# Kernel optimization log

Measured on AMD Instinct MI355X. Metric: run time of the kernel, lower is better.

## Reference

```python
import jax, jax.numpy as jnp
import numpy as np
from jax import lax

FEAT_STRIDE = 16
SCALES = (8.0, 16.0, 32.0)
RATIOS = (0.5, 1.0, 2.0)
PRE_NMS_TOPN = 6000
POST_NMS_TOPN = 300
NMS_THRESH = 0.5
MIN_SIZE = 16.0


def _generate_anchors(base_size=16.0):
    # Faithful Caffe generate_anchors: ratio enumeration outer, scale inner.
    w = h = base_size
    x_ctr = y_ctr = (base_size - 1.0) / 2.0
    size = w * h
    anchors = []
    for r in RATIOS:
        ws = np.round(np.sqrt(size / r))
        hs = np.round(ws * r)
        for s in SCALES:
            W = ws * s
            H = hs * s
            anchors.append([x_ctr - (W - 1) / 2.0, y_ctr - (H - 1) / 2.0,
                            x_ctr + (W - 1) / 2.0, y_ctr + (H - 1) / 2.0])
    return np.asarray(anchors, dtype=np.float32)  # (A=9, 4)


def _nms_keep(boxes, thresh):
    # boxes sorted by descending score; returns bool keep mask. JIT-friendly.
    n = boxes.shape[0]
    x1, y1, x2, y2 = boxes[:, 0], boxes[:, 1], boxes[:, 2], boxes[:, 3]
    areas = (x2 - x1 + 1.0) * (y2 - y1 + 1.0)
    xx1 = jnp.maximum(x1[:, None], x1[None, :])
    yy1 = jnp.maximum(y1[:, None], y1[None, :])
    xx2 = jnp.minimum(x2[:, None], x2[None, :])
    yy2 = jnp.minimum(y2[:, None], y2[None, :])
    inter = jnp.maximum(xx2 - xx1 + 1.0, 0.0) * jnp.maximum(yy2 - yy1 + 1.0, 0.0)
    iou = inter / (areas[:, None] + areas[None, :] - inter)  # (n, n)
    idxs = jnp.arange(n)

    def body(i, keep):
        suppress = (iou[i] > thresh) & keep[i] & (idxs > i)
        return keep & ~suppress

    return lax.fori_loop(0, n, body, jnp.ones((n,), dtype=bool))


def _proposal(scores, bbox_deltas):
    # scores: (1, H, W, 2A) rpn class probs; bbox_deltas: (1, H, W, 4A)
    _, H, W, A4 = bbox_deltas.shape
    A = A4 // 4
    im_h = jnp.float32(H * FEAT_STRIDE)
    im_w = jnp.float32(W * FEAT_STRIDE)

    anchors = jnp.asarray(_generate_anchors())  # (A, 4)
    shift_x = jnp.arange(W, dtype=jnp.float32) * FEAT_STRIDE
    shift_y = jnp.arange(H, dtype=jnp.float32) * FEAT_STRIDE
    sx, sy = jnp.meshgrid(shift_x, shift_y)  # (H, W) row-major like Caffe
    shifts = jnp.stack([sx.ravel(), sy.ravel(), sx.ravel(), sy.ravel()], axis=1)  # (K, 4)
    all_anchors = (anchors[None, :, :] + shifts[:, None, :]).reshape(-1, 4)  # (K*A, 4)

    fg_scores = scores[0, :, :, A:].reshape(-1)        # (K*A,) fg probs
    deltas = bbox_deltas[0].reshape(-1, 4)             # (K*A, 4)

    # bbox_transform_inv (Caffe convention with +1 widths)
    aw = all_anchors[:, 2] - all_anchors[:, 0] + 1.0
    ah = all_anchors[:, 3] - all_anchors[:, 1] + 1.0
    acx = all_anchors[:, 0] + 0.5 * aw
    acy = all_anchors[:, 1] + 0.5 * ah
    dx, dy, dw, dh = deltas[:, 0], deltas[:, 1], deltas[:, 2], deltas[:, 3]
    pcx = dx * aw + acx
    pcy = dy * ah + acy
    pw = jnp.exp(dw) * aw
    ph = jnp.exp(dh) * ah
    x1 = jnp.clip(pcx - 0.5 * pw, 0.0, im_w - 1.0)
    y1 = jnp.clip(pcy - 0.5 * ph, 0.0, im_h - 1.0)
    x2 = jnp.clip(pcx + 0.5 * pw, 0.0, im_w - 1.0)
    y2 = jnp.clip(pcy + 0.5 * ph, 0.0, im_h - 1.0)
    proposals = jnp.stack([x1, y1, x2, y2], axis=1)  # (K*A, 4)

    # min_size filter (im scale = 1): mask score to -inf instead of removing
    ws = x2 - x1 + 1.0
    hs = y2 - y1 + 1.0
    valid = (ws >= MIN_SIZE) & (hs >= MIN_SIZE)
    masked_scores = jnp.where(valid, fg_scores, -jnp.inf)

    top_scores, order = lax.top_k(masked_scores, PRE_NMS_TOPN)
    top_boxes = proposals[order]  # (pre_nms, 4), score-descending

    keep = _nms_keep(lax.stop_gradient(top_boxes), NMS_THRESH)
    keep = keep & jnp.isfinite(top_scores)

    n = PRE_NMS_TOPN
    ranked = jnp.where(keep, jnp.arange(n), n)
    picked = jnp.sort(ranked)[:POST_NMS_TOPN]  # first kept in score order
    ok = picked < n
    picked_c = jnp.minimum(picked, n - 1)
    out_boxes = top_boxes[picked_c] * ok[:, None].astype(top_boxes.dtype)

    # normalized proposals in [0, 1]
    scale = jnp.array([im_w, im_h, im_w, im_h], dtype=top_boxes.dtype)
    return out_boxes / scale  # (post_nms_topN, 4)


def setup_inputs() -> dict:
    key = jax.random.key(0)
    k1, k2 = jax.random.split(key)
    scores = jax.random.uniform(k1, (1, 64, 64, 18), dtype=jnp.float32)
    bbox_deltas = jax.random.normal(k2, (1, 64, 64, 36), dtype=jnp.float32)
    return {"scores": scores, "bbox_deltas": bbox_deltas}


def reference(scores, bbox_deltas):
    return _proposal(scores, bbox_deltas)
```

## Files before the change

### kernel.cpp

```cpp
#include <hip/hip_runtime.h>
#include <math.h>


#define NPROP   36864
#define TOPN    6000
#define POSTN   300
#define NWORDS  94
#define NROUND  47
#define MAXSEL  8192
#define NB      16384
#define NEGINF_PAT 0x007FFFFFu

typedef unsigned long long u64;

__constant__ float ANCH[9][4] = {
    {-84.f,  -40.f,  99.f,  55.f},
    {-176.f, -88.f,  191.f, 103.f},
    {-360.f, -184.f, 375.f, 199.f},
    {-56.f,  -56.f,  71.f,  71.f},
    {-120.f, -120.f, 135.f, 135.f},
    {-248.f, -248.f, 263.f, 263.f},
    {-36.f,  -80.f,  51.f,  95.f},
    {-80.f,  -168.f, 95.f,  183.f},
    {-168.f, -344.f, 183.f, 359.f},
};

__device__ __forceinline__ float4 decode_box(const float* __restrict__ deltas, int i,
                                             bool* valid_out) {
    int a   = i % 9;
    int pos = i / 9;
    int wx = pos & 63, hy = pos >> 6;
    float sx = (float)(wx * 16), sy = (float)(hy * 16);
    float ax1 = ANCH[a][0] + sx, ay1 = ANCH[a][1] + sy;
    float ax2 = ANCH[a][2] + sx, ay2 = ANCH[a][3] + sy;
    float aw  = ax2 - ax1 + 1.0f;
    float ah  = ay2 - ay1 + 1.0f;
    float acx = ax1 + 0.5f * aw;
    float acy = ay1 + 0.5f * ah;
    float4 d4 = ((const float4*)deltas)[i];
    float pcx = __fadd_rn(__fmul_rn(d4.x, aw), acx);
    float pcy = __fadd_rn(__fmul_rn(d4.y, ah), acy);
    float pw  = __fmul_rn(expf(d4.z), aw);
    float ph  = __fmul_rn(expf(d4.w), ah);
    float hx  = __fmul_rn(0.5f, pw);
    float hv  = __fmul_rn(0.5f, ph);
    float x1 = fminf(fmaxf(__fsub_rn(pcx, hx), 0.0f), 1023.0f);
    float y1 = fminf(fmaxf(__fsub_rn(pcy, hv), 0.0f), 1023.0f);
    float x2 = fminf(fmaxf(__fadd_rn(pcx, hx), 0.0f), 1023.0f);
    float y2 = fminf(fmaxf(__fadd_rn(pcy, hv), 0.0f), 1023.0f);
    float bw = __fadd_rn(__fsub_rn(x2, x1), 1.0f);
    float bh = __fadd_rn(__fsub_rn(y2, y1), 1.0f);
    *valid_out = (bw >= 16.0f) && (bh >= 16.0f);
    return make_float4(x1, y1, x2, y2);
}

__device__ __forceinline__ float box_area(float4 b) {
    return __fmul_rn(__fadd_rn(__fsub_rn(b.z, b.x), 1.0f),
                     __fadd_rn(__fsub_rn(b.w, b.y), 1.0f));
}

__global__ __launch_bounds__(256) void decode_kernel(
        const float* __restrict__ scores,
        const float* __restrict__ deltas,
        unsigned* __restrict__ uhigh) {
    int i = blockIdx.x * 256 + threadIdx.x;
    bool valid;
    (void)decode_box(deltas, i, &valid);
    int a = i % 9, pos = i / 9;
    float fg = scores[(size_t)pos * 18 + 9 + a];
    float sc = valid ? fg : -__builtin_huge_valf();
    unsigned u = __float_as_uint(sc);
    u = (u & 0x80000000u) ? ~u : (u | 0x80000000u);
    uhigh[i] = u;
}

__global__ __launch_bounds__(1024) void select_compact(
        const unsigned* __restrict__ uhigh,
        u64* __restrict__ sel,
        unsigned* __restrict__ nsel) {
    __shared__ unsigned h[NB];
    __shared__ unsigned strip[1024];
    __shared__ unsigned thr_sh, cnt_sh;
    int t = threadIdx.x, lane = t & 63, wave = t >> 6;
    #pragma unroll
    for (int r = 0; r < NB / 1024; ++r) h[t + r * 1024] = 0;
    if (t == 0) cnt_sh = 0;
    __syncthreads();

    #pragma unroll
    for (int r = 0; r < 36; ++r) {
        unsigned u = uhigh[t + r * 1024];
        unsigned bkt = u >> 18;
        atomicAdd(&h[(bkt >> 4) + (bkt & 15) * 1024], 1u);
    }
    __syncthreads();

    unsigned s = 0;
    #pragma unroll
    for (int k = 0; k < 16; ++k) s += h[t + k * 1024];
    strip[t] = s;
    __syncthreads();

    if (wave == 0) {
        unsigned g = 0;
        #pragma unroll
        for (int k = 0; k < 16; ++k) g += strip[lane * 16 + k];
        unsigned suf = g;
        #pragma unroll
        for (int off = 1; off < 64; off <<= 1) {
            unsigned x = __shfl_down(suf, off, 64);
            if (lane + off < 64) suf += x;
        }
        u64 bal = __ballot(suf >= TOPN);
        int gsel = 63 - __builtin_clzll(bal);
        unsigned rest = __shfl(suf, (gsel < 63) ? gsel + 1 : 63, 64);
        if (gsel == 63) rest = 0;

        unsigned sv = (lane < 16) ? strip[gsel * 16 + lane] : 0;
        unsigned suf2 = sv;
        #pragma unroll
        for (int off = 1; off < 16; off <<= 1) {
            unsigned x = __shfl_down(suf2, off, 64);
            if (lane + off < 16) suf2 += x;
        }
        u64 bal2 = __ballot((lane < 16) && (rest + suf2 >= TOPN));
        int ssel = 63 - __builtin_clzll(bal2);
        unsigned rest2 = __shfl(suf2, (ssel < 15) ? ssel + 1 : 15, 64);
        if (ssel == 15) rest2 = 0;
        rest2 += rest;
        int S = gsel * 16 + ssel;

        unsigned bv = (lane < 16) ? h[S + lane * 1024] : 0;
        unsigned suf3 = bv;
        #pragma unroll
        for (int off = 1; off < 16; off <<= 1) {
            unsigned x = __shfl_down(suf3, off, 64);
            if (lane + off < 16) suf3 += x;
        }
        u64 bal3 = __ballot((lane < 16) && (rest2 + suf3 >= TOPN));
        int bsel = 63 - __builtin_clzll(bal3);
        if (lane == 0) thr_sh = ((unsigned)(S * 16 + bsel)) << 18;
    }
    __syncthreads();
    unsigned thr = thr_sh;

    for (int r = 0; r < 36; ++r) {
        unsigned u = uhigh[t + r * 1024];
        bool pred = (u >= thr);
        u64 b = __ballot(pred);
        int nb = __popcll(b);
        unsigned base = 0;
        if (lane == 0 && nb) base = atomicAdd(&cnt_sh, (unsigned)nb);
        base = __shfl(base, 0, 64);
        if (pred) {
            unsigned p = base + (unsigned)__popcll(b & ((1ULL << lane) - 1ULL));
            if (p < MAXSEL)
                sel[p] = ((u64)u << 32) |
                         (u64)(0xFFFFFFFFu - (unsigned)(t + r * 1024));
        }
    }
    __syncthreads();
    if (t == 0) *nsel = (cnt_sh > MAXSEL) ? MAXSEL : cnt_sh;
}

__global__ __launch_bounds__(256) void rank_scatter(
        const u64* __restrict__ sel,
        const unsigned* __restrict__ nsel,
        const float* __restrict__ deltas,
        float4* __restrict__ topb,
        float* __restrict__ areas,
        unsigned* __restrict__ topu) {
    __shared__ u64 tile[1024];
    __shared__ int pr[256];
    int t = threadIdx.x;
    int slot = t & 31, seg = t >> 5;
    int n = (int)*nsel; if (n > MAXSEL) n = MAXSEL;
    int j = blockIdx.x * 32 + slot;
    u64 myk = (j < n) ? sel[j] : 0ULL;
    int rk = 0;
    for (int base = 0; base < n; base += 1024) {
        int m = min(1024, n - base);
        for (int q = t; q < m; q += 256) tile[q] = sel[base + q];
        __syncthreads();
        for (int q = seg; q < m; q += 8) rk += (tile[q] > myk) ? 1 : 0;
        __syncthreads();
    }
    pr[seg * 32 + slot] = rk;
    __syncthreads();
    if (t < 32) {
        int jj = blockIdx.x * 32 + t;
        int rtot = 0;
        #pragma unroll
        for (int s2 = 0; s2 < 8; ++s2) rtot += pr[s2 * 32 + t];
        if (jj < n && rtot < TOPN) {
            u64 k = sel[jj];
            unsigned idx = 0xFFFFFFFFu - (unsigned)(k & 0xFFFFFFFFull);
            bool valid;
            float4 b = decode_box(deltas, (int)idx, &valid);
            topb[rtot]  = b;
            areas[rtot] = box_area(b);
            topu[rtot]  = (unsigned)(k >> 32);
        }
    }
}

__global__ void nms_mask(const float4* __restrict__ boxes,
                         const float* __restrict__ areas,
                         u64* __restrict__ mask) {
    int rb = blockIdx.x, cb = blockIdx.y;
    if (cb < rb) return;
    __shared__ float4 cbx[64];
    __shared__ float  car[64];
    int tid = threadIdx.x;
    int j0 = cb * 64;
    if (j0 + tid < TOPN) { cbx[tid] = boxes[j0 + tid]; car[tid] = areas[j0 + tid]; }
    __syncthreads();
    int i = rb * 64 + tid;
    if (i >= TOPN) return;
    float4 bi = boxes[i];
    float  ai = areas[i];
    u64 bits = 0ULL;
    int jmax = min(64, TOPN - j0);
    for (int jj = 0; jj < jmax; ++jj) {
        int j = j0 + jj;
        if (j <= i) continue;
        float4 bj = cbx[jj];
        float xx1 = fmaxf(bi.x, bj.x);
        float yy1 = fmaxf(bi.y, bj.y);
        float xx2 = fminf(bi.z, bj.z);
        float yy2 = fminf(bi.w, bj.w);
        float w = fmaxf(__fadd_rn(__fsub_rn(xx2, xx1), 1.0f), 0.0f);
        float h = fmaxf(__fadd_rn(__fsub_rn(yy2, yy1), 1.0f), 0.0f);
        float inter = __fmul_rn(w, h);
        float denom = __fsub_rn(__fadd_rn(ai, car[jj]), inter);
        float iou = inter / denom;
        if (iou > 0.5f) bits |= (1ULL << jj);
    }
    mask[(size_t)i * NWORDS + cb] = bits;
}

__global__ __launch_bounds__(1024) void nms_scan(
        const u64* __restrict__ mask,
        const unsigned* __restrict__ topu,
        const float4* __restrict__ topb,
        float* __restrict__ out) {
    __shared__ unsigned rem32[NWORDS * 2];
    __shared__ u64 diag[2][128][4];
    __shared__ u64 Fsh[2][2];
    __shared__ short kept_rows[2][128];
    __shared__ short kept_list[POSTN];
    __shared__ int nk_sh[2];
    __shared__ int cnt_sh, stop_sh;

    int t = threadIdx.x, wave = t >> 6, lane = t & 63;
    if (t >= 640 && t < 640 + NWORDS * 2) rem32[t - 640] = 0;
    if (t >= 128 && t < 640) {
        int idx = t - 128;
        diag[0][idx >> 2][idx & 3] = mask[(size_t)(idx >> 2) * NWORDS + (idx & 3)];
    }
    if (wave == 0) {
        u64 f = __ballot(topu[lane] != NEGINF_PAT);
        if (lane == 0) { Fsh[0][0] = f; cnt_sh = 0; stop_sh = 0; nk_sh[0] = 0; nk_sh[1] = 0; }
    } else if (wave == 1) {
        u64 f = __ballot(topu[64 + lane] != NEGINF_PAT);
        if (lane == 0) Fsh[0][1] = f;
    }
    __syncthreads();

    u64 urg0 = 0, urg1 = 0;

    for (int r = 0; r < NROUND; ++r) {
        int p = r & 1;
        int i0 = r * 128;
        if (wave == 0) {
            u64 r0w0 = diag[p][lane][0];
            u64 r0w1 = diag[p][lane][1];
            u64 r1w1 = diag[p][64 + lane][1];
            u64 R0 = ((u64)rem32[4 * r]     | ((u64)rem32[4 * r + 1] << 32)) | urg0;
            u64 R1 = ((u64)rem32[4 * r + 2] | ((u64)rem32[4 * r + 3] << 32)) | urg1;
            int nb = min(128, TOPN - i0);
            u64 v1 = (nb >= 128) ? ~0ULL : ((1ULL << (nb - 64)) - 1ULL);
            u64 a0 = ~R0;
            u64 a1 = ~R1 & v1;
            u64 k0 = 0ULL, k1 = 0ULL;
            while (a0) {
                int ii = __builtin_ctzll(a0);
                u64 bit = 1ULL << ii;
                k0 |= bit;
                u64 s0 = __shfl(r0w0, ii, 64);
                u64 s1 = __shfl(r0w1, ii, 64);
                a0 &= ~(s0 | bit);
                a1 &= ~s1;
            }
            while (a1) {
                int ii = __builtin_ctzll(a1);
                u64 bit = 1ULL << ii;
                k1 |= bit;
                u64 s1 = __shfl(r1w1, ii, 64);
                a1 &= ~(s1 | bit);
            }
            u64 F0 = Fsh[p][0], F1 = Fsh[p][1];
            u64 kf0 = k0 & F0, kf1 = k1 & F1;
            int nk0 = __popcll(k0);
            int c0  = __popcll(kf0);
            int base = cnt_sh;
            u64 ltm = (1ULL << lane) - 1ULL;
            if ((k0 >> lane) & 1)
                kept_rows[p][__popcll(k0 & ltm)] = (short)(i0 + lane);
            if ((k1 >> lane) & 1)
                kept_rows[p][nk0 + __popcll(k1 & ltm)] = (short)(i0 + 64 + lane);
            if ((kf0 >> lane) & 1) {
                int pos = base + __popcll(kf0 & ltm);
                if (pos < POSTN) kept_list[pos] = (short)(i0 + lane);
            }
            if ((kf1 >> lane) & 1) {
                int pos = base + c0 + __popcll(kf1 & ltm);
                if (pos < POSTN) kept_list[pos] = (short)(i0 + 64 + lane);
            }
            u64 a0u = 0ULL, a1u = 0ULL;
            if ((k0 >> lane) & 1) { a0u = diag[p][lane][2];       a1u = diag[p][lane][3]; }
            if ((k1 >> lane) & 1) { a0u |= diag[p][64 + lane][2]; a1u |= diag[p][64 + lane][3]; }
            #pragma unroll
            for (int off = 1; off < 64; off <<= 1) {
                a0u |= __shfl_xor(a0u, off, 64);
                a1u |= __shfl_xor(a1u, off, 64);
            }
            urg0 = a0u; urg1 = a1u;
            if (lane == 0) {
                nk_sh[p] = nk0 + __popcll(k1);
                int cc = base + c0 + __popcll(kf1);
                if (cc > POSTN) cc = POSTN;
                cnt_sh = cc;
                stop_sh = (cc >= POSTN) || (r == NROUND - 1);
            }
        } else if (wave == 15) {
            if (r + 1 < NROUND) {
                int i1 = i0 + 128;
                #pragma unroll
                for (int q = lane; q < 512; q += 64) {
                    int row = i1 + (q >> 2), k = q & 3;
                    int wd = 2 * (r + 1) + k;
                    diag[p ^ 1][q >> 2][k] = (row < TOPN && wd < NWORDS)
                        ? mask[(size_t)row * NWORDS + wd] : 0ULL;
                }
                u64 fa = __ballot((i1 + lane < TOPN) && (topu[i1 + lane] != NEGINF_PAT));
                u64 fb = __ballot((i1 + 64 + lane < TOPN) && (topu[i1 + 64 + lane] != NEGINF_PAT));
                if (lane == 0) { Fsh[p ^ 1][0] = fa; Fsh[p ^ 1][1] = fb; }
            }
        } else {
            int nkp = nk_sh[p ^ 1];
            int left = NWORDS - (2 * r + 2);
            if (r > 0 && nkp > 0 && left > 0) {
                int tot = nkp * left;
                for (int q = t - 64; q < tot; q += 896) {
                    int k  = q / left;
                    int wd = 2 * r + 2 + (q - k * left);
                    int row = kept_rows[p ^ 1][k];
                    u64 v = mask[(size_t)row * NWORDS + wd];
                    if (v) {
                        unsigned lo = (unsigned)v, hi = (unsigned)(v >> 32);
                        if (lo) atomicOr(&rem32[2 * wd],     lo);
                        if (hi) atomicOr(&rem32[2 * wd + 1], hi);
                    }
                }
            }
        }
        __syncthreads();
        if (stop_sh) break;
    }

    if (t < POSTN) {
        float4 v = make_float4(0.f, 0.f, 0.f, 0.f);
        if (t < cnt_sh) {
            float4 b = topb[kept_list[t]];
            const float s = 0.0009765625f;
            v = make_float4(b.x * s, b.y * s, b.z * s, b.w * s);
        }
        ((float4*)out)[t] = v;
    }
}

extern "C" void kernel_launch(void* const* d_in, const int* in_sizes, int n_in,
                              void* d_out, int out_size, void* d_ws, size_t ws_size,
                              hipStream_t stream) {
    const float* scores = (const float*)d_in[0];
    const float* deltas = (const float*)d_in[1];
    float* out = (float*)d_out;

    char* w = (char*)d_ws;
    unsigned* uhigh = (unsigned*)(w);
    u64*      sel   = (u64*)(w + 147456);
    unsigned* nsel  = (unsigned*)(w + 212992);
    float4*   topb  = (float4*)(w + 213008);
    float*    areas = (float*)(w + 309008);
    unsigned* topu  = (unsigned*)(w + 333008);
    u64*      mask  = (u64*)(w + 357008);

    decode_kernel<<<NPROP / 256, 256, 0, stream>>>(scores, deltas, uhigh);
    select_compact<<<1, 1024, 0, stream>>>(uhigh, sel, nsel);
    rank_scatter<<<MAXSEL / 32, 256, 0, stream>>>(sel, nsel, deltas, topb, areas, topu);
    nms_mask<<<dim3(NWORDS, NWORDS), 64, 0, stream>>>(topb, areas, mask);
    nms_scan<<<1, 1024, 0, stream>>>(mask, topu, topb, out);
}
```

Measured before the change: 175.6 us.

## Fuse decode and select kernels via last-block spin wait; simplify rank scatter

Merges the decode kernel and the single-block top-k selection into one launch. Each of the 36 blocks decodes and writes its keys, then publishes a done flag, and the last block spins on all flags before running the histogram select. This removes one kernel launch and its gap. Separately, rank_scatter now gives each thread one candidate and has it scan the whole selected list alone, dropping the 8-way split and the shared-memory reduction. That serialises more compare work per thread on only 32 blocks. The done flags are never reset, so a later call could read stale values and skip the wait.

```diff
diff --git a/kernel.cpp b/kernel.cpp
--- a/kernel.cpp
+++ b/kernel.cpp
@@ -9,6 +9,8 @@
 #define NROUND  47
 #define MAXSEL  8192
 #define NB      16384
+#define NDBLK   36
+#define MAGIC   0x13572468u
 #define NEGINF_PAT 0x007FFFFFu
 
 typedef unsigned long long u64;
@@ -59,34 +61,49 @@
                      __fadd_rn(__fsub_rn(b.w, b.y), 1.0f));
 }
 
-__global__ __launch_bounds__(256) void decode_kernel(
+__global__ __launch_bounds__(1024) void decode_select(
         const float* __restrict__ scores,
         const float* __restrict__ deltas,
-        unsigned* __restrict__ uhigh) {
-    int i = blockIdx.x * 256 + threadIdx.x;
-    bool valid;
-    (void)decode_box(deltas, i, &valid);
-    int a = i % 9, pos = i / 9;
-    float fg = scores[(size_t)pos * 18 + 9 + a];
-    float sc = valid ? fg : -__builtin_huge_valf();
-    unsigned u = __float_as_uint(sc);
-    u = (u & 0x80000000u) ? ~u : (u | 0x80000000u);
-    uhigh[i] = u;
-}
-
-__global__ __launch_bounds__(1024) void select_compact(
-        const unsigned* __restrict__ uhigh,
+        unsigned* __restrict__ uhigh,
+        unsigned* __restrict__ done,
         u64* __restrict__ sel,
         unsigned* __restrict__ nsel) {
     __shared__ unsigned h[NB];
     __shared__ unsigned strip[1024];
     __shared__ unsigned thr_sh, cnt_sh;
     int t = threadIdx.x, lane = t & 63, wave = t >> 6;
+    int b = blockIdx.x;
+    int i = b * 1024 + t;
+
+    bool valid;
+    (void)decode_box(deltas, i, &valid);
+    {
+        int a = i % 9, pos = i / 9;
+        float fg = scores[(size_t)pos * 18 + 9 + a];
+        float sc = valid ? fg : -__builtin_huge_valf();
+        unsigned u = __float_as_uint(sc);
+        u = (u & 0x80000000u) ? ~u : (u | 0x80000000u);
+        uhigh[i] = u;
+    }
+    __threadfence();
+    __syncthreads();
+    if (t == 0)
+        __hip_atomic_store(&done[b], MAGIC, __ATOMIC_RELEASE,
+                           __HIP_MEMORY_SCOPE_AGENT);
+    if (b != NDBLK - 1) return;
+
+    if (t == 0) {
+        for (int k = 0; k < NDBLK; ++k)
+            while (__hip_atomic_load(&done[k], __ATOMIC_ACQUIRE,
+                                     __HIP_MEMORY_SCOPE_AGENT) != MAGIC) { }
+    }
+    __syncthreads();
+    __threadfence();
+
     #pragma unroll
     for (int r = 0; r < NB / 1024; ++r) h[t + r * 1024] = 0;
     if (t == 0) cnt_sh = 0;
     __syncthreads();
-
     #pragma unroll
     for (int r = 0; r < 36; ++r) {
         unsigned u = uhigh[t + r * 1024];
@@ -147,13 +164,13 @@
     for (int r = 0; r < 36; ++r) {
         unsigned u = uhigh[t + r * 1024];
         bool pred = (u >= thr);
-        u64 b = __ballot(pred);
-        int nb = __popcll(b);
+        u64 bal = __ballot(pred);
+        int nb = __popcll(bal);
         unsigned base = 0;
         if (lane == 0 && nb) base = atomicAdd(&cnt_sh, (unsigned)nb);
         base = __shfl(base, 0, 64);
         if (pred) {
-            unsigned p = base + (unsigned)__popcll(b & ((1ULL << lane) - 1ULL));
+            unsigned p = base + (unsigned)__popcll(bal & ((1ULL << lane) - 1ULL));
             if (p < MAXSEL)
                 sel[p] = ((u64)u << 32) |
                          (u64)(0xFFFFFFFFu - (unsigned)(t + r * 1024));
@@ -171,36 +188,26 @@
         float* __restrict__ areas,
         unsigned* __restrict__ topu) {
     __shared__ u64 tile[1024];
-    __shared__ int pr[256];
     int t = threadIdx.x;
-    int slot = t & 31, seg = t >> 5;
+    int j = blockIdx.x * 256 + t;
     int n = (int)*nsel; if (n > MAXSEL) n = MAXSEL;
-    int j = blockIdx.x * 32 + slot;
     u64 myk = (j < n) ? sel[j] : 0ULL;
     int rk = 0;
     for (int base = 0; base < n; base += 1024) {
         int m = min(1024, n - base);
         for (int q = t; q < m; q += 256) tile[q] = sel[base + q];
         __syncthreads();
-        for (int q = seg; q < m; q += 8) rk += (tile[q] > myk) ? 1 : 0;
+        #pragma unroll 4
+        for (int q = 0; q < m; ++q) rk += (tile[q] > myk) ? 1 : 0;
         __syncthreads();
     }
-    pr[seg * 32 + slot] = rk;
-    __syncthreads();
-    if (t < 32) {
-        int jj = blockIdx.x * 32 + t;
-        int rtot = 0;
-        #pragma unroll
-        for (int s2 = 0; s2 < 8; ++s2) rtot += pr[s2 * 32 + t];
-        if (jj < n && rtot < TOPN) {
-            u64 k = sel[jj];
-            unsigned idx = 0xFFFFFFFFu - (unsigned)(k & 0xFFFFFFFFull);
-            bool valid;
-            float4 b = decode_box(deltas, (int)idx, &valid);
-            topb[rtot]  = b;
-            areas[rtot] = box_area(b);
-            topu[rtot]  = (unsigned)(k >> 32);
-        }
+    if (j < n && rk < TOPN) {
+        unsigned idx = 0xFFFFFFFFu - (unsigned)(myk & 0xFFFFFFFFull);
+        bool valid;
+        float4 b = decode_box(deltas, (int)idx, &valid);
+        topb[rk]  = b;
+        areas[rk] = box_area(b);
+        topu[rk]  = (unsigned)(myk >> 32);
     }
 }
 
@@ -391,14 +398,14 @@
     unsigned* uhigh = (unsigned*)(w);
     u64*      sel   = (u64*)(w + 147456);
     unsigned* nsel  = (unsigned*)(w + 212992);
-    float4*   topb  = (float4*)(w + 213008);
-    float*    areas = (float*)(w + 309008);
-    unsigned* topu  = (unsigned*)(w + 333008);
-    u64*      mask  = (u64*)(w + 357008);
-
-    decode_kernel<<<NPROP / 256, 256, 0, stream>>>(scores, deltas, uhigh);
-    select_compact<<<1, 1024, 0, stream>>>(uhigh, sel, nsel);
-    rank_scatter<<<MAXSEL / 32, 256, 0, stream>>>(sel, nsel, deltas, topb, areas, topu);
+    unsigned* done  = (unsigned*)(w + 213008);
+    float4*   topb  = (float4*)(w + 213152);
+    float*    areas = (float*)(w + 309152);
+    unsigned* topu  = (unsigned*)(w + 333152);
+    u64*      mask  = (u64*)(w + 357152);
+
+    decode_select<<<NDBLK, 1024, 0, stream>>>(scores, deltas, uhigh, done, sel, nsel);
+    rank_scatter<<<MAXSEL / 256, 256, 0, stream>>>(sel, nsel, deltas, topb, areas, topu);
     nms_mask<<<dim3(NWORDS, NWORDS), 64, 0, stream>>>(topb, areas, mask);
     nms_scan<<<1, 1024, 0, stream>>>(mask, topu, topb, out);
 }
```

Result: slower. 261.6 us (+48.9%).
